# Performance work log

Measured on AMD Instinct MI355X. Metric: run time of the kernel, lower is better.

Reference implementation:

```python
import jax, jax.numpy as jnp
import numpy as np

N_NODES = 40000
N_EDGES = 640000
IN_DIM = 128
HID = 128
N_GRAPHS = 256
N_CLASSES = 1


def setup_inputs() -> dict:
    key = jax.random.key(0)
    ks = jax.random.split(key, 16)
    h = jax.random.normal(ks[0], (N_NODES, IN_DIM), dtype=jnp.float32)
    src = jax.random.randint(ks[1], (N_EDGES,), 0, N_NODES, dtype=jnp.int32)
    dst = jax.random.randint(ks[2], (N_EDGES,), 0, N_NODES, dtype=jnp.int32)
    graph_ids = jnp.sort(jax.random.randint(ks[3], (N_NODES,), 0, N_GRAPHS, dtype=jnp.int32))
    s = 1.0 / np.sqrt(HID)
    W1 = jax.random.normal(ks[4], (IN_DIM, HID), dtype=jnp.float32) * s
    b1 = jnp.zeros((HID,), jnp.float32)
    W2 = jax.random.normal(ks[5], (HID, HID), dtype=jnp.float32) * s
    b2 = jnp.zeros((HID,), jnp.float32)
    Wc1 = jax.random.normal(ks[6], (HID, HID), dtype=jnp.float32) * s
    bc1 = jnp.zeros((HID,), jnp.float32)
    Wc2 = jax.random.normal(ks[7], (HID, HID), dtype=jnp.float32) * s
    bc2 = jnp.zeros((HID,), jnp.float32)
    Wc3 = jax.random.normal(ks[8], (HID, N_CLASSES), dtype=jnp.float32) * s
    bc3 = jnp.zeros((N_CLASSES,), jnp.float32)
    return dict(h=h, src=src, dst=dst, graph_ids=graph_ids,
                W1=W1, b1=b1, W2=W2, b2=b2,
                Wc1=Wc1, bc1=bc1, Wc2=Wc2, bc2=bc2, Wc3=Wc3, bc3=bc3)


def _graph_conv(h, src, dst, W, b):
    # DGL GraphConv with norm='both': out = D_in^{-1/2} A D_out^{-1/2} h W + b
    ones = jnp.ones((src.shape[0],), h.dtype)
    deg_out = jax.ops.segment_sum(ones, src, num_segments=N_NODES)
    deg_in = jax.ops.segment_sum(ones, dst, num_segments=N_NODES)
    norm_s = jnp.clip(deg_out, 1.0, None) ** -0.5  # [N]
    norm_d = jnp.clip(deg_in, 1.0, None) ** -0.5
    # mult weight first (in_dim >= out_dim path in DGL); math identical either way
    hw = (h * norm_s[:, None]) @ W                  # [N, HID]
    agg = jax.ops.segment_sum(hw[src], dst, num_segments=N_NODES)  # gather-scatter
    return agg * norm_d[:, None] + b


def reference(h, src, dst, graph_ids, W1, b1, W2, b2, Wc1, bc1, Wc2, bc2, Wc3, bc3):
    h1 = jax.nn.relu(_graph_conv(h, src, dst, W1, b1))
    h1 = jax.nn.relu(_graph_conv(h1, src, dst, W2, b2))
    # dgl.mean_nodes: per-graph mean over nodes
    sums = jax.ops.segment_sum(h1, graph_ids, num_segments=N_GRAPHS)      # [G, HID]
    counts = jax.ops.segment_sum(jnp.ones((N_NODES,), h1.dtype), graph_ids,
                                 num_segments=N_GRAPHS)
    hg = sums / jnp.maximum(counts, 1.0)[:, None]
    out = jax.nn.relu(hg @ Wc1 + bc1)
    out = jax.nn.relu(out @ Wc2 + bc2)
    return out @ Wc3 + bc3
```

## Files before the change

kernel.cpp:

```cpp
#include <hip/hip_runtime.h>

#define HID 128
#define CAP 64
#define HBLK 160
#define PERIOD 21

typedef unsigned int uint;
typedef unsigned short ushort;

typedef __attribute__((ext_vector_type(8))) short short8;
typedef __attribute__((ext_vector_type(4))) float floatx4;

static __device__ __forceinline__ ushort f2bf(float f) {
    uint u = __float_as_uint(f);
    u += 0x7fffu + ((u >> 16) & 1u);
    return (ushort)(u >> 16);
}
static __device__ __forceinline__ float bf2f(ushort v) {
    return __uint_as_float(((uint)v) << 16);
}

__global__ void gc_wpack(const float* __restrict__ W1, const float* __restrict__ W2,
                         uint4* __restrict__ wpk) {
    int which = blockIdx.x;
    const float* W = which ? W2 : W1;
    uint4* o = wpk + (size_t)which * 2048;
    for (int i = threadIdx.x; i < 2048; i += 256) {
        int lane = i & 63;
        int kc = (i >> 6) & 3;
        int nt = i >> 8;
        int n = nt * 16 + (lane & 15);
        int k0 = kc * 32 + (lane >> 4) * 8;
        uint p[4];
        #pragma unroll
        for (int j = 0; j < 4; ++j) {
            ushort a = f2bf(W[(size_t)(k0 + 2 * j) * HID + n]);
            ushort b = f2bf(W[(size_t)(k0 + 2 * j + 1) * HID + n]);
            p[j] = (uint)a | ((uint)b << 16);
        }
        uint4 v; v.x = p[0]; v.y = p[1]; v.z = p[2]; v.w = p[3];
        o[i] = v;
    }
}

__global__ void gc_build_mm(const int* __restrict__ src, const int* __restrict__ dst,
                            int* __restrict__ cnt_in, ushort* __restrict__ slot,
                            uint* __restrict__ pblock,
                            const float* __restrict__ X, const uint4* __restrict__ wpk,
                            ushort* __restrict__ hw, int n_edges, int n_nodes) {
    __shared__ uint hb4[10000];
    int b = blockIdx.x;
    int r = b % PERIOD, q = b / PERIOD;
    int t = threadIdx.x;

    if (r < 16) {
        int bi = q * 16 + r;
        if (bi >= 2500) return;
        int e = bi * 256 + t;
        if (e < n_edges) {
            int s = src[e], d = dst[e];
            int pos = atomicAdd(&cnt_in[d], 1);
            if (pos < CAP) slot[(size_t)d * CAP + pos] = (ushort)s;
        }
    } else if (r == 16) {
        int hq = q;
        if (hq >= HBLK) return;
        for (int i = t; i < 10000; i += 256) hb4[i] = 0u;
        __syncthreads();
        int per = (n_edges + HBLK - 1) / HBLK;
        int e0 = hq * per, e1 = min(e0 + per, n_edges);
        for (int e = e0 + t; e < e1; e += 256) {
            int s = src[e];
            atomicAdd(&hb4[s >> 2], 1u << ((s & 3) * 8));
        }
        __syncthreads();
        uint* o = pblock + (size_t)hq * 10000;
        for (int i = t; i < 10000; i += 256) o[i] = hb4[i];
    } else {
        int mb = q * 4 + (r - 17);
        if (mb >= 625) return;
        int wave = (mb * 256 + t) >> 6;
        int lane = t & 63;
        int tiles = n_nodes >> 4;
        if (wave >= tiles) return;
        int m = lane & 15, quad = lane >> 4;
        int node = wave * 16 + m;
        const float* xrow = X + (size_t)node * HID;

        floatx4 acc[8];
        #pragma unroll
        for (int nt = 0; nt < 8; ++nt) acc[nt] = (floatx4){0.f, 0.f, 0.f, 0.f};

        #pragma unroll
        for (int kc = 0; kc < 4; ++kc) {
            const float4 xa = *reinterpret_cast<const float4*>(xrow + kc * 32 + quad * 8);
            const float4 xb = *reinterpret_cast<const float4*>(xrow + kc * 32 + quad * 8 + 4);
            uint4 xu;
            xu.x = (uint)f2bf(xa.x) | ((uint)f2bf(xa.y) << 16);
            xu.y = (uint)f2bf(xa.z) | ((uint)f2bf(xa.w) << 16);
            xu.z = (uint)f2bf(xb.x) | ((uint)f2bf(xb.y) << 16);
            xu.w = (uint)f2bf(xb.z) | ((uint)f2bf(xb.w) << 16);
            short8 xf = *reinterpret_cast<short8*>(&xu);
            #pragma unroll
            for (int nt = 0; nt < 8; ++nt) {
                uint4 wu = wpk[(size_t)(nt * 4 + kc) * 64 + lane];
                short8 wf = *reinterpret_cast<short8*>(&wu);
                acc[nt] = __builtin_amdgcn_mfma_f32_16x16x32_bf16(wf, xf, acc[nt], 0, 0, 0);
            }
        }
        #pragma unroll
        for (int nt = 0; nt < 8; ++nt) {
            uint2 v;
            v.x = (uint)f2bf(acc[nt][0]) | ((uint)f2bf(acc[nt][1]) << 16);
            v.y = (uint)f2bf(acc[nt][2]) | ((uint)f2bf(acc[nt][3]) << 16);
            *reinterpret_cast<uint2*>(hw + (size_t)node * HID + nt * 16 + quad * 4) = v;
        }
    }
}

__global__ void gc_reduce(const uint* __restrict__ pblock, int* __restrict__ cnt_out,
                          int n_nodes) {
    int i = blockIdx.x * blockDim.x + threadIdx.x;
    if (i >= 10000) return;
    uint a0 = 0, a1 = 0, a2 = 0, a3 = 0;
    for (int b = 0; b < HBLK; ++b) {
        uint v = pblock[(size_t)b * 10000 + i];
        a0 += v & 0xffu;
        a1 += (v >> 8) & 0xffu;
        a2 += (v >> 16) & 0xffu;
        a3 += v >> 24;
    }
    int4 o; o.x = (int)a0; o.y = (int)a1; o.z = (int)a2; o.w = (int)a3;
    *reinterpret_cast<int4*>(cnt_out + i * 4) = o;
}

__global__ void gc_gather_mm(const ushort* __restrict__ HW, const int* __restrict__ cnt_in,
                             const int* __restrict__ cnt_out, const ushort* __restrict__ slot,
                             const float* __restrict__ b, const uint4* __restrict__ wpk2,
                             ushort* __restrict__ hw2, int n_nodes) {
    __shared__ ushort tile[16 * HID];
    int tid = threadIdx.x;
    int ts = tid >> 4;
    int l16 = tid & 15;
    int node = blockIdx.x * 16 + ts;
    int q = l16 << 3;

    int ci = cnt_in[node];
    int cnt = min(ci, CAP);
    const ushort* row = slot + (size_t)node * CAP;
    float a[8];
    #pragma unroll
    for (int j = 0; j < 8; ++j) a[j] = 0.0f;

    auto accum = [&](uint4 u, float ns) {
        a[0] = fmaf(ns, __uint_as_float(u.x << 16), a[0]);
        a[1] = fmaf(ns, __uint_as_float(u.x & 0xffff0000u), a[1]);
        a[2] = fmaf(ns, __uint_as_float(u.y << 16), a[2]);
        a[3] = fmaf(ns, __uint_as_float(u.y & 0xffff0000u), a[3]);
        a[4] = fmaf(ns, __uint_as_float(u.z << 16), a[4]);
        a[5] = fmaf(ns, __uint_as_float(u.z & 0xffff0000u), a[5]);
        a[6] = fmaf(ns, __uint_as_float(u.w << 16), a[6]);
        a[7] = fmaf(ns, __uint_as_float(u.w & 0xffff0000u), a[7]);
    };

    int e = 0;
    for (; e + 3 < cnt; e += 4) {
        int s0 = row[e], s1 = row[e + 1], s2 = row[e + 2], s3 = row[e + 3];
        uint4 u0 = *reinterpret_cast<const uint4*>(HW + (size_t)s0 * HID + q);
        uint4 u1 = *reinterpret_cast<const uint4*>(HW + (size_t)s1 * HID + q);
        uint4 u2 = *reinterpret_cast<const uint4*>(HW + (size_t)s2 * HID + q);
        uint4 u3 = *reinterpret_cast<const uint4*>(HW + (size_t)s3 * HID + q);
        float n0 = rsqrtf(fmaxf((float)cnt_out[s0], 1.0f));
        float n1 = rsqrtf(fmaxf((float)cnt_out[s1], 1.0f));
        float n2 = rsqrtf(fmaxf((float)cnt_out[s2], 1.0f));
        float n3 = rsqrtf(fmaxf((float)cnt_out[s3], 1.0f));
        accum(u0, n0); accum(u1, n1); accum(u2, n2); accum(u3, n3);
    }
    for (; e < cnt; ++e) {
        int s0 = row[e];
        uint4 u0 = *reinterpret_cast<const uint4*>(HW + (size_t)s0 * HID + q);
        accum(u0, rsqrtf(fmaxf((float)cnt_out[s0], 1.0f)));
    }

    float nd = rsqrtf(fmaxf((float)ci, 1.0f));
    const float4 bv0 = *reinterpret_cast<const float4*>(b + q);
    const float4 bv1 = *reinterpret_cast<const float4*>(b + q + 4);
    float r[8];
    r[0] = fmaxf(a[0] * nd + bv0.x, 0.0f);
    r[1] = fmaxf(a[1] * nd + bv0.y, 0.0f);
    r[2] = fmaxf(a[2] * nd + bv0.z, 0.0f);
    r[3] = fmaxf(a[3] * nd + bv0.w, 0.0f);
    r[4] = fmaxf(a[4] * nd + bv1.x, 0.0f);
    r[5] = fmaxf(a[5] * nd + bv1.y, 0.0f);
    r[6] = fmaxf(a[6] * nd + bv1.z, 0.0f);
    r[7] = fmaxf(a[7] * nd + bv1.w, 0.0f);
    uint4 v;
    v.x = (uint)f2bf(r[0]) | ((uint)f2bf(r[1]) << 16);
    v.y = (uint)f2bf(r[2]) | ((uint)f2bf(r[3]) << 16);
    v.z = (uint)f2bf(r[4]) | ((uint)f2bf(r[5]) << 16);
    v.w = (uint)f2bf(r[6]) | ((uint)f2bf(r[7]) << 16);
    *reinterpret_cast<uint4*>(&tile[ts * HID + ((l16 ^ ts) << 3)]) = v;
    __syncthreads();

    int wv = tid >> 6;
    int lane = tid & 63;
    int m = lane & 15, quad = lane >> 4;
    int onode = blockIdx.x * 16 + m;

    floatx4 acc0 = (floatx4){0.f, 0.f, 0.f, 0.f};
    floatx4 acc1 = (floatx4){0.f, 0.f, 0.f, 0.f};
    int nt0 = wv * 2, nt1 = wv * 2 + 1;
    #pragma unroll
    for (int kc = 0; kc < 4; ++kc) {
        int cc = (kc * 4 + quad) ^ m;
        uint4 xu = *reinterpret_cast<const uint4*>(&tile[m * HID + (cc << 3)]);
        short8 xf = *reinterpret_cast<short8*>(&xu);
        uint4 w0 = wpk2[(size_t)(nt0 * 4 + kc) * 64 + lane];
        uint4 w1 = wpk2[(size_t)(nt1 * 4 + kc) * 64 + lane];
        short8 wf0 = *reinterpret_cast<short8*>(&w0);
        short8 wf1 = *reinterpret_cast<short8*>(&w1);
        acc0 = __builtin_amdgcn_mfma_f32_16x16x32_bf16(wf0, xf, acc0, 0, 0, 0);
        acc1 = __builtin_amdgcn_mfma_f32_16x16x32_bf16(wf1, xf, acc1, 0, 0, 0);
    }
    float ns = rsqrtf(fmaxf((float)cnt_out[onode], 1.0f));
    {
        uint2 o0, o1;
        o0.x = (uint)f2bf(acc0[0] * ns) | ((uint)f2bf(acc0[1] * ns) << 16);
        o0.y = (uint)f2bf(acc0[2] * ns) | ((uint)f2bf(acc0[3] * ns) << 16);
        o1.x = (uint)f2bf(acc1[0] * ns) | ((uint)f2bf(acc1[1] * ns) << 16);
        o1.y = (uint)f2bf(acc1[2] * ns) | ((uint)f2bf(acc1[3] * ns) << 16);
        *reinterpret_cast<uint2*>(hw2 + (size_t)onode * HID + nt0 * 16 + quad * 4) = o0;
        *reinterpret_cast<uint2*>(hw2 + (size_t)onode * HID + nt1 * 16 + quad * 4) = o1;
    }
}

__global__ void gc_gather(const ushort* __restrict__ HW, const int* __restrict__ cnt_in,
                          const ushort* __restrict__ slot,
                          const float* __restrict__ b, ushort* __restrict__ out,
                          int n_nodes) {
    int node = blockIdx.x * 16 + (threadIdx.x >> 4);
    if (node >= n_nodes) return;
    int q = (threadIdx.x & 15) << 3;
    int ci = cnt_in[node];
    int cnt = min(ci, CAP);
    const ushort* row = slot + (size_t)node * CAP;
    float a[8];
    #pragma unroll
    for (int j = 0; j < 8; ++j) a[j] = 0.0f;

    auto accum = [&](uint4 u) {
        a[0] += __uint_as_float(u.x << 16);
        a[1] += __uint_as_float(u.x & 0xffff0000u);
        a[2] += __uint_as_float(u.y << 16);
        a[3] += __uint_as_float(u.y & 0xffff0000u);
        a[4] += __uint_as_float(u.z << 16);
        a[5] += __uint_as_float(u.z & 0xffff0000u);
        a[6] += __uint_as_float(u.w << 16);
        a[7] += __uint_as_float(u.w & 0xffff0000u);
    };

    int e = 0;
    for (; e + 3 < cnt; e += 4) {
        int s0 = row[e], s1 = row[e + 1], s2 = row[e + 2], s3 = row[e + 3];
        uint4 u0 = *reinterpret_cast<const uint4*>(HW + (size_t)s0 * HID + q);
        uint4 u1 = *reinterpret_cast<const uint4*>(HW + (size_t)s1 * HID + q);
        uint4 u2 = *reinterpret_cast<const uint4*>(HW + (size_t)s2 * HID + q);
        uint4 u3 = *reinterpret_cast<const uint4*>(HW + (size_t)s3 * HID + q);
        accum(u0); accum(u1); accum(u2); accum(u3);
    }
    for (; e < cnt; ++e) {
        uint4 u0 = *reinterpret_cast<const uint4*>(HW + (size_t)row[e] * HID + q);
        accum(u0);
    }

    float nd = rsqrtf(fmaxf((float)ci, 1.0f));
    const float4 bv0 = *reinterpret_cast<const float4*>(b + q);
    const float4 bv1 = *reinterpret_cast<const float4*>(b + q + 4);
    float r[8];
    r[0] = fmaxf(a[0] * nd + bv0.x, 0.0f);
    r[1] = fmaxf(a[1] * nd + bv0.y, 0.0f);
    r[2] = fmaxf(a[2] * nd + bv0.z, 0.0f);
    r[3] = fmaxf(a[3] * nd + bv0.w, 0.0f);
    r[4] = fmaxf(a[4] * nd + bv1.x, 0.0f);
    r[5] = fmaxf(a[5] * nd + bv1.y, 0.0f);
    r[6] = fmaxf(a[6] * nd + bv1.z, 0.0f);
    r[7] = fmaxf(a[7] * nd + bv1.w, 0.0f);
    uint4 v;
    v.x = (uint)f2bf(r[0]) | ((uint)f2bf(r[1]) << 16);
    v.y = (uint)f2bf(r[2]) | ((uint)f2bf(r[3]) << 16);
    v.z = (uint)f2bf(r[4]) | ((uint)f2bf(r[5]) << 16);
    v.w = (uint)f2bf(r[6]) | ((uint)f2bf(r[7]) << 16);
    *reinterpret_cast<uint4*>(out + (size_t)node * HID + q) = v;
}

__global__ void gc_pool_part(const ushort* __restrict__ h2, const int* __restrict__ gid,
                             int n_nodes, float* __restrict__ part) {
    int g = blockIdx.x >> 3;
    int k = blockIdx.x & 7;
    int t = threadIdx.x;
    int half = t >> 7, c = t & 127;
    int beg, end;
    {
        int lo = 0, hi = n_nodes;
        while (lo < hi) { int mid = (lo + hi) >> 1; if (gid[mid] < g) lo = mid + 1; else hi = mid; }
        beg = lo;
        lo = beg; hi = n_nodes;
        while (lo < hi) { int mid = (lo + hi) >> 1; if (gid[mid] < g + 1) lo = mid + 1; else hi = mid; }
        end = lo;
    }
    float s = 0.0f;
    for (int i = beg + k * 2 + half; i < end; i += 16)
        s += bf2f(h2[(size_t)i * HID + c]);
    __shared__ float sh[2][HID];
    sh[half][c] = s;
    __syncthreads();
    if (half == 0) part[(size_t)blockIdx.x * HID + c] = sh[0][c] + sh[1][c];
}

__global__ void gc_mlp(const float* __restrict__ part, const int* __restrict__ gid,
                       int n_nodes,
                       const float* __restrict__ Wc1, const float* __restrict__ bc1,
                       const float* __restrict__ Wc2, const float* __restrict__ bc2,
                       const float* __restrict__ Wc3, const float* __restrict__ bc3,
                       float* __restrict__ out) {
    int g = blockIdx.x;
    int c = threadIdx.x;
    int beg, end;
    {
        int lo = 0, hi = n_nodes;
        while (lo < hi) { int mid = (lo + hi) >> 1; if (gid[mid] < g) lo = mid + 1; else hi = mid; }
        beg = lo;
        lo = beg; hi = n_nodes;
        while (lo < hi) { int mid = (lo + hi) >> 1; if (gid[mid] < g + 1) lo = mid + 1; else hi = mid; }
        end = lo;
    }
    float s = 0.0f;
    #pragma unroll
    for (int k = 0; k < 8; ++k) s += part[(size_t)(g * 8 + k) * HID + c];
    float inv = 1.0f / fmaxf((float)(end - beg), 1.0f);
    __shared__ float x[HID];
    __shared__ float y[HID];
    __shared__ float red[HID];
    x[c] = s * inv;
    __syncthreads();
    float a = bc1[c];
    for (int k = 0; k < HID; ++k) a += x[k] * Wc1[(size_t)k * HID + c];
    y[c] = fmaxf(a, 0.0f);
    __syncthreads();
    float a2 = bc2[c];
    for (int k = 0; k < HID; ++k) a2 += y[k] * Wc2[(size_t)k * HID + c];
    float z = fmaxf(a2, 0.0f);
    red[c] = z * Wc3[c];
    __syncthreads();
    for (int sr = 64; sr > 0; sr >>= 1) {
        if (c < sr) red[c] += red[c + sr];
        __syncthreads();
    }
    if (c == 0) out[g] = red[0] + bc3[0];
}

extern "C" void kernel_launch(void* const* d_in, const int* in_sizes, int n_in,
                              void* d_out, int out_size, void* d_ws, size_t ws_size,
                              hipStream_t stream) {
    const float* h    = (const float*)d_in[0];
    const int*   src  = (const int*)d_in[1];
    const int*   dst  = (const int*)d_in[2];
    const int*   gid  = (const int*)d_in[3];
    const float* W1   = (const float*)d_in[4];
    const float* b1   = (const float*)d_in[5];
    const float* W2   = (const float*)d_in[6];
    const float* b2   = (const float*)d_in[7];
    const float* Wc1  = (const float*)d_in[8];
    const float* bc1  = (const float*)d_in[9];
    const float* Wc2  = (const float*)d_in[10];
    const float* bc2  = (const float*)d_in[11];
    const float* Wc3  = (const float*)d_in[12];
    const float* bc3  = (const float*)d_in[13];
    float* out = (float*)d_out;

    const int n_nodes  = in_sizes[0] / HID;
    const int n_edges  = in_sizes[1];
    const int n_graphs = 256;

    char* wsb = (char*)d_ws;
    size_t off = 0;
    auto alloc = [&](size_t bytes) {
        void* p = wsb + off;
        off += (bytes + 15) & ~(size_t)15;
        return p;
    };

    int*    cnt_out = (int*)alloc((size_t)n_nodes * 4);
    int*    cnt_in  = (int*)alloc((size_t)n_nodes * 4);
    ushort* slot    = (ushort*)alloc((size_t)n_nodes * CAP * 2);
    uint*   pblock  = (uint*)alloc((size_t)HBLK * 10000 * 4);
    float*  ppart   = (float*)alloc((size_t)n_graphs * 8 * HID * 4);
    uint4*  wpk     = (uint4*)alloc((size_t)2 * 2048 * 16);
    ushort* hw      = (ushort*)alloc((size_t)n_nodes * HID * 2);
    ushort* hw2     = (ushort*)alloc((size_t)n_nodes * HID * 2);
    ushort* h2      = hw;

    hipMemsetAsync(cnt_in, 0, (size_t)n_nodes * sizeof(int), stream);

    gc_wpack<<<2, 256, 0, stream>>>(W1, W2, wpk);

    gc_build_mm<<<PERIOD * 160, 256, 0, stream>>>(src, dst, cnt_in, slot, pblock,
                                                  h, wpk, hw, n_edges, n_nodes);
    gc_reduce<<<(10000 + 255) / 256, 256, 0, stream>>>(pblock, cnt_out, n_nodes);

    const int ga_grid = n_nodes / 16;

    gc_gather_mm<<<ga_grid, 256, 0, stream>>>(hw, cnt_in, cnt_out, slot, b1,
                                              wpk + 2048, hw2, n_nodes);
    gc_gather<<<ga_grid, 256, 0, stream>>>(hw2, cnt_in, slot, b2, h2, n_nodes);

    gc_pool_part<<<n_graphs * 8, 256, 0, stream>>>(h2, gid, n_nodes, ppart);
    gc_mlp<<<n_graphs, HID, 0, stream>>>(ppart, gid, n_nodes,
                                         Wc1, bc1, Wc2, bc2, Wc3, bc3, out);
}
```

Baseline: 213.8 us.

## Batch edge work per thread, halve histogram LDS, precompute source norms, deepen gather unroll

The build kernel now processes four edges per thread in the slot-fill role, which cuts that role's block count and shrinks the interleave period. The histogram role splits the node range into two passes over a 20KB shared array, trading a second pass over src for lower LDS use and higher occupancy. gc_reduce now writes rsqrt-normalized source degrees, so the gather kernels load a precomputed float instead of recomputing rsqrt per edge. The gather loops are unrolled by 8 to put more independent loads in flight, at the cost of more registers.

```diff
diff --git a/kernel.cpp b/kernel.cpp
--- a/kernel.cpp
+++ b/kernel.cpp
@@ -3,7 +3,7 @@
 #define HID 128
 #define CAP 64
 #define HBLK 160
-#define PERIOD 21
+#define PERIOD 9
 
 typedef unsigned int uint;
 typedef unsigned short ushort;
@@ -48,36 +48,48 @@
                             uint* __restrict__ pblock,
                             const float* __restrict__ X, const uint4* __restrict__ wpk,
                             ushort* __restrict__ hw, int n_edges, int n_nodes) {
-    __shared__ uint hb4[10000];
+    __shared__ uint hb4[5000];
     int b = blockIdx.x;
     int r = b % PERIOD, q = b / PERIOD;
     int t = threadIdx.x;
 
-    if (r < 16) {
-        int bi = q * 16 + r;
-        if (bi >= 2500) return;
-        int e = bi * 256 + t;
-        if (e < n_edges) {
-            int s = src[e], d = dst[e];
-            int pos = atomicAdd(&cnt_in[d], 1);
-            if (pos < CAP) slot[(size_t)d * CAP + pos] = (ushort)s;
+    if (r < 4) {
+        int bi = q * 4 + r;
+        if (bi >= 625) return;
+        int e0 = bi * 1024 + t;
+        int s[4], d[4], p[4];
+        #pragma unroll
+        for (int j = 0; j < 4; ++j) {
+            int e = e0 + j * 256;
+            s[j] = src[e];
+            d[j] = dst[e];
         }
-    } else if (r == 16) {
+        #pragma unroll
+        for (int j = 0; j < 4; ++j) p[j] = atomicAdd(&cnt_in[d[j]], 1);
+        #pragma unroll
+        for (int j = 0; j < 4; ++j)
+            if (p[j] < CAP) slot[(size_t)d[j] * CAP + p[j]] = (ushort)s[j];
+    } else if (r == 4) {
         int hq = q;
         if (hq >= HBLK) return;
-        for (int i = t; i < 10000; i += 256) hb4[i] = 0u;
-        __syncthreads();
         int per = (n_edges + HBLK - 1) / HBLK;
         int e0 = hq * per, e1 = min(e0 + per, n_edges);
-        for (int e = e0 + t; e < e1; e += 256) {
-            int s = src[e];
-            atomicAdd(&hb4[s >> 2], 1u << ((s & 3) * 8));
+        #pragma unroll
+        for (int c = 0; c < 2; ++c) {
+            int lo = c * 20000;
+            for (int i = t; i < 5000; i += 256) hb4[i] = 0u;
+            __syncthreads();
+            for (int e = e0 + t; e < e1; e += 256) {
+                int s = src[e] - lo;
+                if ((unsigned)s < 20000u) atomicAdd(&hb4[s >> 2], 1u << ((s & 3) * 8));
+            }
+            __syncthreads();
+            uint* o = pblock + (size_t)hq * 10000 + c * 5000;
+            for (int i = t; i < 5000; i += 256) o[i] = hb4[i];
+            __syncthreads();
         }
-        __syncthreads();
-        uint* o = pblock + (size_t)hq * 10000;
-        for (int i = t; i < 10000; i += 256) o[i] = hb4[i];
     } else {
-        int mb = q * 4 + (r - 17);
+        int mb = q * 4 + (r - 5);
         if (mb >= 625) return;
         int wave = (mb * 256 + t) >> 6;
         int lane = t & 63;
@@ -118,7 +130,7 @@
     }
 }
 
-__global__ void gc_reduce(const uint* __restrict__ pblock, int* __restrict__ cnt_out,
+__global__ void gc_reduce(const uint* __restrict__ pblock, float* __restrict__ norm_s,
                           int n_nodes) {
     int i = blockIdx.x * blockDim.x + threadIdx.x;
     if (i >= 10000) return;
@@ -130,12 +142,16 @@
         a2 += (v >> 16) & 0xffu;
         a3 += v >> 24;
     }
-    int4 o; o.x = (int)a0; o.y = (int)a1; o.z = (int)a2; o.w = (int)a3;
-    *reinterpret_cast<int4*>(cnt_out + i * 4) = o;
+    float4 o;
+    o.x = rsqrtf(fmaxf((float)a0, 1.0f));
+    o.y = rsqrtf(fmaxf((float)a1, 1.0f));
+    o.z = rsqrtf(fmaxf((float)a2, 1.0f));
+    o.w = rsqrtf(fmaxf((float)a3, 1.0f));
+    *reinterpret_cast<float4*>(norm_s + i * 4) = o;
 }
 
 __global__ void gc_gather_mm(const ushort* __restrict__ HW, const int* __restrict__ cnt_in,
-                             const int* __restrict__ cnt_out, const ushort* __restrict__ slot,
+                             const float* __restrict__ norm_s, const ushort* __restrict__ slot,
                              const float* __restrict__ b, const uint4* __restrict__ wpk2,
                              ushort* __restrict__ hw2, int n_nodes) {
     __shared__ ushort tile[16 * HID];
@@ -164,22 +180,22 @@
     };
 
     int e = 0;
-    for (; e + 3 < cnt; e += 4) {
-        int s0 = row[e], s1 = row[e + 1], s2 = row[e + 2], s3 = row[e + 3];
-        uint4 u0 = *reinterpret_cast<const uint4*>(HW + (size_t)s0 * HID + q);
-        uint4 u1 = *reinterpret_cast<const uint4*>(HW + (size_t)s1 * HID + q);
-        uint4 u2 = *reinterpret_cast<const uint4*>(HW + (size_t)s2 * HID + q);
-        uint4 u3 = *reinterpret_cast<const uint4*>(HW + (size_t)s3 * HID + q);
-        float n0 = rsqrtf(fmaxf((float)cnt_out[s0], 1.0f));
-        float n1 = rsqrtf(fmaxf((float)cnt_out[s1], 1.0f));
-        float n2 = rsqrtf(fmaxf((float)cnt_out[s2], 1.0f));
-        float n3 = rsqrtf(fmaxf((float)cnt_out[s3], 1.0f));
-        accum(u0, n0); accum(u1, n1); accum(u2, n2); accum(u3, n3);
+    for (; e + 7 < cnt; e += 8) {
+        int s[8]; uint4 u[8]; float ns[8];
+        #pragma unroll
+        for (int j = 0; j < 8; ++j) s[j] = row[e + j];
+        #pragma unroll
+        for (int j = 0; j < 8; ++j)
+            u[j] = *reinterpret_cast<const uint4*>(HW + (size_t)s[j] * HID + q);
+        #pragma unroll
+        for (int j = 0; j < 8; ++j) ns[j] = norm_s[s[j]];
+        #pragma unroll
+        for (int j = 0; j < 8; ++j) accum(u[j], ns[j]);
     }
     for (; e < cnt; ++e) {
         int s0 = row[e];
         uint4 u0 = *reinterpret_cast<const uint4*>(HW + (size_t)s0 * HID + q);
-        accum(u0, rsqrtf(fmaxf((float)cnt_out[s0], 1.0f)));
+        accum(u0, norm_s[s0]);
     }
 
     float nd = rsqrtf(fmaxf((float)ci, 1.0f));
@@ -222,7 +238,7 @@
         acc0 = __builtin_amdgcn_mfma_f32_16x16x32_bf16(wf0, xf, acc0, 0, 0, 0);
         acc1 = __builtin_amdgcn_mfma_f32_16x16x32_bf16(wf1, xf, acc1, 0, 0, 0);
     }
-    float ns = rsqrtf(fmaxf((float)cnt_out[onode], 1.0f));
+    float ns = norm_s[onode];
     {
         uint2 o0, o1;
         o0.x = (uint)f2bf(acc0[0] * ns) | ((uint)f2bf(acc0[1] * ns) << 16);
@@ -260,13 +276,15 @@
     };
 
     int e = 0;
-    for (; e + 3 < cnt; e += 4) {
-        int s0 = row[e], s1 = row[e + 1], s2 = row[e + 2], s3 = row[e + 3];
-        uint4 u0 = *reinterpret_cast<const uint4*>(HW + (size_t)s0 * HID + q);
-        uint4 u1 = *reinterpret_cast<const uint4*>(HW + (size_t)s1 * HID + q);
-        uint4 u2 = *reinterpret_cast<const uint4*>(HW + (size_t)s2 * HID + q);
-        uint4 u3 = *reinterpret_cast<const uint4*>(HW + (size_t)s3 * HID + q);
-        accum(u0); accum(u1); accum(u2); accum(u3);
+    for (; e + 7 < cnt; e += 8) {
+        int s[8]; uint4 u[8];
+        #pragma unroll
+        for (int j = 0; j < 8; ++j) s[j] = row[e + j];
+        #pragma unroll
+        for (int j = 0; j < 8; ++j)
+            u[j] = *reinterpret_cast<const uint4*>(HW + (size_t)s[j] * HID + q);
+        #pragma unroll
+        for (int j = 0; j < 8; ++j) accum(u[j]);
     }
     for (; e < cnt; ++e) {
         uint4 u0 = *reinterpret_cast<const uint4*>(HW + (size_t)row[e] * HID + q);
@@ -390,7 +408,7 @@
         return p;
     };
 
-    int*    cnt_out = (int*)alloc((size_t)n_nodes * 4);
+    float*  norm_s  = (float*)alloc((size_t)n_nodes * 4);
     int*    cnt_in  = (int*)alloc((size_t)n_nodes * 4);
     ushort* slot    = (ushort*)alloc((size_t)n_nodes * CAP * 2);
     uint*   pblock  = (uint*)alloc((size_t)HBLK * 10000 * 4);
@@ -406,11 +424,11 @@
 
     gc_build_mm<<<PERIOD * 160, 256, 0, stream>>>(src, dst, cnt_in, slot, pblock,
                                                   h, wpk, hw, n_edges, n_nodes);
-    gc_reduce<<<(10000 + 255) / 256, 256, 0, stream>>>(pblock, cnt_out, n_nodes);
+    gc_reduce<<<(10000 + 255) / 256, 256, 0, stream>>>(pblock, norm_s, n_nodes);
 
     const int ga_grid = n_nodes / 16;
 
-    gc_gather_mm<<<ga_grid, 256, 0, stream>>>(hw, cnt_in, cnt_out, slot, b1,
+    gc_gather_mm<<<ga_grid, 256, 0, stream>>>(hw, cnt_in, norm_s, slot, b1,
                                               wpk + 2048, hw2, n_nodes);
     gc_gather<<<ga_grid, 256, 0, stream>>>(hw2, cnt_in, slot, b2, h2, n_nodes);
 
```

New measurement: 219.8 us. +2.8%, slower.
